# Optimization experiments

Measured on AMD Instinct MI355X. Metric: run time of the kernel, lower is better.

The kernel has to match this reference:

```python
import jax, jax.numpy as jnp
import numpy as np


def setup_inputs() -> dict:
    key = jax.random.key(0)
    k1, k2 = jax.random.split(key)
    T, D, K = 100000, 768, 500  # frames, feature dim (HuBERT base), k-means clusters
    feat = jax.random.normal(k1, (T, D), dtype=jnp.float32)
    C = jax.random.normal(k2, (D, K), dtype=jnp.float32)  # cluster centers, transposed as in module
    return {"feat": feat, "C": C}


def reference(feat, C):
    # Squared euclidean distance expanded: ||f||^2 - 2 f.C + ||c||^2
    Cnorm = jnp.sum(C * C, axis=0, keepdims=True)            # [1, K]
    fnorm = jnp.sum(feat * feat, axis=1, keepdims=True)       # [T, 1]
    dist = fnorm - 2.0 * jnp.matmul(feat, C) + Cnorm          # [T, K]
    return jnp.argmin(dist, axis=1)[None, :]                  # [1, T] cluster ids
```

## Files before the change

kernel.cpp:

```cpp
#include <hip/hip_runtime.h>
#include <float.h>

#define D_DIM 768
#define K_DIM 500
#define NDT   24
#define BM    64
#define NTH   512
#define PB_STRIDE 100352

typedef _Float16 f16x8 __attribute__((ext_vector_type(8)));
typedef _Float16 f16x4 __attribute__((ext_vector_type(4)));
typedef float    f32x4 __attribute__((ext_vector_type(4)));


__global__ void cnorm_partial_kernel(const float* __restrict__ C,
                                     double* __restrict__ partial, int K) {
    const int k = threadIdx.x;
    const int w = blockIdx.x;
    double s = 0.0;
    if (k < K) {
        const int d0 = w * (D_DIM / 16);
        for (int d = d0; d < d0 + (D_DIM / 16); ++d) {
            const float c = C[(size_t)d * K + k];
            s = fma((double)c, (double)c, s);
        }
    }
    partial[w * 512 + k] = s;
}

__global__ void cnorm_finish_kernel(const double* __restrict__ partial,
                                    float* __restrict__ cnorm, int K) {
    const int k = threadIdx.x;
    if (k < K) {
        double s = 0.0;
        for (int w = 0; w < 16; ++w) s += partial[w * 512 + k];
        cnorm[k] = (float)s;
    } else {
        cnorm[k] = FLT_MAX;
    }
}

__global__ void packB_kernel(const float* __restrict__ C,
                             _Float16* __restrict__ BpH,
                             _Float16* __restrict__ BpL) {
    const int idx = blockIdx.x * 256 + threadIdx.x;
    const int col = idx & 511;
    const int dt  = idx >> 9;
    f16x8 h[4], l[4];
    #pragma unroll
    for (int c = 0; c < 4; ++c)
        #pragma unroll
        for (int j = 0; j < 8; ++j) {
            const int k = c * 8 + j;
            const float v = (col < K_DIM)
                          ? C[(size_t)(dt * 32 + k) * K_DIM + col] : 0.0f;
            const _Float16 hh = (_Float16)v;
            h[c][j] = hh;
            l[c][j] = (_Float16)(v - (float)hh);
        }
    f16x8* dH = (f16x8*)(BpH + ((size_t)dt * 512 + col) * 32);
    f16x8* dL = (f16x8*)(BpL + ((size_t)dt * 512 + col) * 32);
    #pragma unroll
    for (int c = 0; c < 4; ++c) { dH[c] = h[c]; dL[c] = l[c]; }
}

__launch_bounds__(NTH, 4)
__global__ void assign_kernel(const float* __restrict__ feat,
                              const _Float16* __restrict__ BpH,
                              const _Float16* __restrict__ BpL,
                              const float* __restrict__ cnorm,
                              float* __restrict__ pbv,
                              int* __restrict__ pbi,
                              int T) {
    __shared__ __align__(16) _Float16 AsH[2][BM * 32];
    __shared__ __align__(16) _Float16 AsL[2][BM * 32];
    __shared__ float red_v[BM * 8];
    __shared__ int   red_i[BM * 8];

    const int tid  = threadIdx.x;
    const int wn   = tid >> 6;
    const int lane = tid & 63;
    const int l15  = lane & 15;
    const int kg   = lane >> 4;
    const int bid  = blockIdx.x;
    const int half = bid & 1;
    const int R0   = (bid >> 1) * BM;

    const int ar = tid >> 3;
    const int jj = tid & 7;
    const bool arow_ok = (R0 + ar) < T;
    const float* fptr = feat + (size_t)(R0 + ar) * D_DIM + jj * 4;
    const int aslot = (((jj >> 1) + (ar >> 1)) & 3);
    const int aoff  = ar * 32 + aslot * 8 + (jj & 1) * 4;

    const int colbase = half * 256 + wn * 32 + l15;
    const _Float16* bpH = BpH + (size_t)colbase * 32 + kg * 8;
    const _Float16* bpL = BpL + (size_t)colbase * 32 + kg * 8;

    f32x4 acc[4][2];
    #pragma unroll
    for (int m = 0; m < 4; ++m)
        #pragma unroll
        for (int n = 0; n < 2; ++n) acc[m][n] = (f32x4){0.f, 0.f, 0.f, 0.f};

#define CVT_STORE(V, BUF) do {                                                 \
    const float fa_[4] = {(V).x, (V).y, (V).z, (V).w};                         \
    f16x4 h_, l_;                                                              \
    _Pragma("unroll")                                                          \
    for (int j = 0; j < 4; ++j) {                                              \
        const _Float16 hh = (_Float16)fa_[j];                                  \
        h_[j] = hh; l_[j] = (_Float16)(fa_[j] - (float)hh);                    \
    }                                                                          \
    *(f16x4*)(AsH[BUF] + aoff) = h_;                                           \
    *(f16x4*)(AsL[BUF] + aoff) = l_;                                           \
} while (0)

#define SOFT_BARRIER() do {                                                    \
    asm volatile("s_waitcnt lgkmcnt(0)" ::: "memory");                         \
    __builtin_amdgcn_s_barrier();                                              \
} while (0)

#define BODY(DT, BCH, BCL, BNH, BNL, ACUR, ANXT) do {                          \
    const int cur = (DT) & 1;                                                  \
           \
    if ((DT) + 1 < NDT) {                                                      \
        const size_t bo1 = (size_t)((DT) + 1) * 16384;                         \
        BNH[0] = *(const f16x8*)(bpH + bo1);                                   \
        BNH[1] = *(const f16x8*)(bpH + bo1 + 512);                             \
        BNL[0] = *(const f16x8*)(bpL + bo1);                                   \
        BNL[1] = *(const f16x8*)(bpL + bo1 + 512);                             \
    }                                                                          \
                                                     \
    if ((DT) + 2 < NDT && arow_ok) {                                           \
        ANXT = *(const float4*)(fptr + ((DT) + 2) * 32);                       \
    }                                                                          \
                                            \
    f16x8 aH[4], aL[4];                                                        \
    _Pragma("unroll")                                                          \
    for (int m = 0; m < 4; ++m) {                                              \
        const int row = m * 16 + l15;                                          \
        const int sl  = (kg + (row >> 1)) & 3;                                 \
        aH[m] = ((const f16x8*)AsH[cur])[row * 4 + sl];                        \
        aL[m] = ((const f16x8*)AsL[cur])[row * 4 + sl];                        \
    }                                                                          \
         \
    __builtin_amdgcn_s_setprio(1);                                             \
    _Pragma("unroll")                                                          \
    for (int nh = 0; nh < 2; ++nh)                                             \
        _Pragma("unroll")                                                      \
        for (int m = 0; m < 4; ++m) {                                          \
            f32x4 a = acc[m][nh];                                              \
            a = __builtin_amdgcn_mfma_f32_16x16x32_f16(aH[m], BCH[nh], a, 0, 0, 0); \
            a = __builtin_amdgcn_mfma_f32_16x16x32_f16(aL[m], BCH[nh], a, 0, 0, 0); \
            a = __builtin_amdgcn_mfma_f32_16x16x32_f16(aH[m], BCL[nh], a, 0, 0, 0); \
            acc[m][nh] = a;                                                    \
        }                                                                      \
    __builtin_amdgcn_s_setprio(0);                                             \
                  \
    if ((DT) + 1 < NDT) {                                                      \
        CVT_STORE(ACUR, cur ^ 1);                                              \
    }                                                                          \
    SOFT_BARRIER();                                                            \
} while (0)

    {
        float4 v = make_float4(0.f, 0.f, 0.f, 0.f);
        if (arow_ok) v = *(const float4*)(fptr);
        CVT_STORE(v, 0);
    }
    f16x8 bAH[2], bAL[2], bBH[2], bBL[2];
    bAH[0] = *(const f16x8*)(bpH);
    bAH[1] = *(const f16x8*)(bpH + 512);
    bAL[0] = *(const f16x8*)(bpL);
    bAL[1] = *(const f16x8*)(bpL + 512);
    float4 avA = make_float4(0.f, 0.f, 0.f, 0.f), avB = avA;
    if (arow_ok) avA = *(const float4*)(fptr + 32);
    SOFT_BARRIER();

    for (int it2 = 0; it2 < NDT; it2 += 2) {
        BODY(it2,     bAH, bAL, bBH, bBL, avA, avB);
        BODY(it2 + 1, bBH, bBL, bAH, bAL, avB, avA);
    }
#undef BODY
#undef SOFT_BARRIER
#undef CVT_STORE

    float cn[2];
    #pragma unroll
    for (int nh = 0; nh < 2; ++nh)
        cn[nh] = cnorm[half * 256 + wn * 32 + nh * 16 + l15];

    #pragma unroll
    for (int m = 0; m < 4; ++m) {
        #pragma unroll
        for (int r = 0; r < 4; ++r) {
            float best = cn[0] - 2.0f * acc[m][0][r];
            int   bi   = colbase;
            {
                const int col = colbase + 16;
                const float s = cn[1] - 2.0f * acc[m][1][r];
                if (s < best || (s == best && col < bi)) { best = s; bi = col; }
            }
            #pragma unroll
            for (int msk = 1; msk < 16; msk <<= 1) {
                const float ov = __shfl_xor(best, msk, 64);
                const int   oi = __shfl_xor(bi,   msk, 64);
                if (ov < best || (ov == best && oi < bi)) { best = ov; bi = oi; }
            }
            if (l15 == 0) {
                const int rl = m * 16 + kg * 4 + r;
                red_v[rl * 8 + wn] = best;
                red_i[rl * 8 + wn] = bi;
            }
        }
    }
    __syncthreads();

    if (tid < BM) {
        float bv = red_v[tid * 8];
        int   bi = red_i[tid * 8];
        #pragma unroll
        for (int w = 1; w < 8; ++w) {
            const float v = red_v[tid * 8 + w];
            const int   i = red_i[tid * 8 + w];
            if (v < bv || (v == bv && i < bi)) { bv = v; bi = i; }
        }
        const int r = R0 + tid;
        if (r < T) {
            pbv[(size_t)half * PB_STRIDE + r] = bv;
            pbi[(size_t)half * PB_STRIDE + r] = bi;
        }
    }
}

__global__ void combine_kernel(const float* __restrict__ pbv,
                               const int* __restrict__ pbi,
                               int* __restrict__ out, int T) {
    const int r = blockIdx.x * 256 + threadIdx.x;
    if (r < T) {
        const float s0 = pbv[r];
        const int   i0 = pbi[r];
        const float s1 = pbv[PB_STRIDE + r];
        const int   i1 = pbi[PB_STRIDE + r];
        out[r] = (s1 < s0) ? i1 : i0;
    }
}

extern "C" void kernel_launch(void* const* d_in, const int* in_sizes, int n_in,
                              void* d_out, int out_size, void* d_ws, size_t ws_size,
                              hipStream_t stream) {
    const float* feat = (const float*)d_in[0];
    const float* C    = (const float*)d_in[1];
    int* out          = (int*)d_out;
    const int T = in_sizes[0] / D_DIM;
    const int K = in_sizes[1] / D_DIM;

    float*     cnorm   = (float*)d_ws;
    double*    partial = (double*)((char*)d_ws + 4096);
    _Float16*  BpH     = (_Float16*)((char*)d_ws + 131072);
    _Float16*  BpL     = (_Float16*)((char*)d_ws + 917504);
    float*     pbv     = (float*)((char*)d_ws + 1703936);
    int*       pbi     = (int*)((char*)d_ws + 2506752);

    hipLaunchKernelGGL(cnorm_partial_kernel, dim3(16), dim3(512), 0, stream,
                       C, partial, K);
    hipLaunchKernelGGL(cnorm_finish_kernel, dim3(1), dim3(512), 0, stream,
                       partial, cnorm, K);
    hipLaunchKernelGGL(packB_kernel, dim3(48), dim3(256), 0, stream,
                       C, BpH, BpL);

    const int nrb = (T + BM - 1) / BM;
    hipLaunchKernelGGL(assign_kernel, dim3(nrb * 2), dim3(NTH), 0, stream,
                       feat, BpH, BpL, cnorm, pbv, pbi, T);
    hipLaunchKernelGGL(combine_kernel, dim3((T + 255) / 256), dim3(256), 0, stream,
                       pbv, pbi, out, T);
}
```

Before: 297.5 us.

## Cover all 512 columns per block, drop column split and combine kernel

Each block now handles all 512 padded centroid columns (each wave 64 columns, 4 MFMA column tiles) instead of splitting columns across two blocks. This halves redundant feature loads and fp16 split conversions per row and removes the partial-result buffers and the separate combine kernel launch. B fragments are now loaded within the same iteration instead of being prefetched one step ahead, and the occupancy hint drops from 4 to 3 blocks per CU because the larger accumulator array needs more registers. Both changes may expose B load latency.

New measurement: 342.5 us. +15.1%, slower.

```diff
diff --git a/kernel.cpp b/kernel.cpp
--- a/kernel.cpp
+++ b/kernel.cpp
@@ -6,7 +6,6 @@
 #define NDT   24
 #define BM    64
 #define NTH   512
-#define PB_STRIDE 100352
 
 typedef _Float16 f16x8 __attribute__((ext_vector_type(8)));
 typedef _Float16 f16x4 __attribute__((ext_vector_type(4)));
@@ -64,13 +63,12 @@
     for (int c = 0; c < 4; ++c) { dH[c] = h[c]; dL[c] = l[c]; }
 }
 
-__launch_bounds__(NTH, 4)
+__launch_bounds__(NTH, 3)
 __global__ void assign_kernel(const float* __restrict__ feat,
                               const _Float16* __restrict__ BpH,
                               const _Float16* __restrict__ BpL,
                               const float* __restrict__ cnorm,
-                              float* __restrict__ pbv,
-                              int* __restrict__ pbi,
+                              int* __restrict__ out,
                               int T) {
     __shared__ __align__(16) _Float16 AsH[2][BM * 32];
     __shared__ __align__(16) _Float16 AsL[2][BM * 32];
@@ -82,9 +80,7 @@
     const int lane = tid & 63;
     const int l15  = lane & 15;
     const int kg   = lane >> 4;
-    const int bid  = blockIdx.x;
-    const int half = bid & 1;
-    const int R0   = (bid >> 1) * BM;
+    const int R0   = blockIdx.x * BM;
 
     const int ar = tid >> 3;
     const int jj = tid & 7;
@@ -93,15 +89,15 @@
     const int aslot = (((jj >> 1) + (ar >> 1)) & 3);
     const int aoff  = ar * 32 + aslot * 8 + (jj & 1) * 4;
 
-    const int colbase = half * 256 + wn * 32 + l15;
+    const int colbase = wn * 64 + l15;
     const _Float16* bpH = BpH + (size_t)colbase * 32 + kg * 8;
     const _Float16* bpL = BpL + (size_t)colbase * 32 + kg * 8;
 
-    f32x4 acc[4][2];
+    f32x4 acc[4][4];
     #pragma unroll
     for (int m = 0; m < 4; ++m)
         #pragma unroll
-        for (int n = 0; n < 2; ++n) acc[m][n] = (f32x4){0.f, 0.f, 0.f, 0.f};
+        for (int n = 0; n < 4; ++n) acc[m][n] = (f32x4){0.f, 0.f, 0.f, 0.f};
 
 #define CVT_STORE(V, BUF) do {                                                 \
     const float fa_[4] = {(V).x, (V).y, (V).z, (V).w};                         \
@@ -120,19 +116,20 @@
     __builtin_amdgcn_s_barrier();                                              \
 } while (0)
 
-#define BODY(DT, BCH, BCL, BNH, BNL, ACUR, ANXT) do {                          \
+#define BODY(DT, CUR, NXT) do {                                                \
     const int cur = (DT) & 1;                                                  \
-           \
-    if ((DT) + 1 < NDT) {                                                      \
-        const size_t bo1 = (size_t)((DT) + 1) * 16384;                         \
-        BNH[0] = *(const f16x8*)(bpH + bo1);                                   \
-        BNH[1] = *(const f16x8*)(bpH + bo1 + 512);                             \
-        BNL[0] = *(const f16x8*)(bpL + bo1);                                   \
-        BNL[1] = *(const f16x8*)(bpL + bo1 + 512);                             \
-    }                                                                          \
-                                                     \
+         \
+       \
+    const size_t bo = (size_t)(DT) * 16384;                                    \
+    f16x8 bH[4], bL[4];                                                        \
+    _Pragma("unroll")                                                          \
+    for (int nh = 0; nh < 4; ++nh) {                                           \
+        bH[nh] = *(const f16x8*)(bpH + bo + nh * 512);                         \
+        bL[nh] = *(const f16x8*)(bpL + bo + nh * 512);                         \
+    }                                                                          \
+          \
     if ((DT) + 2 < NDT && arow_ok) {                                           \
-        ANXT = *(const float4*)(fptr + ((DT) + 2) * 32);                       \
+        NXT = *(const float4*)(fptr + ((DT) + 2) * 32);                        \
     }                                                                          \
                                             \
     f16x8 aH[4], aL[4];                                                        \
@@ -143,22 +140,21 @@
         aH[m] = ((const f16x8*)AsH[cur])[row * 4 + sl];                        \
         aL[m] = ((const f16x8*)AsL[cur])[row * 4 + sl];                        \
     }                                                                          \
-         \
     __builtin_amdgcn_s_setprio(1);                                             \
     _Pragma("unroll")                                                          \
-    for (int nh = 0; nh < 2; ++nh)                                             \
+    for (int nh = 0; nh < 4; ++nh)                                             \
         _Pragma("unroll")                                                      \
         for (int m = 0; m < 4; ++m) {                                          \
             f32x4 a = acc[m][nh];                                              \
-            a = __builtin_amdgcn_mfma_f32_16x16x32_f16(aH[m], BCH[nh], a, 0, 0, 0); \
-            a = __builtin_amdgcn_mfma_f32_16x16x32_f16(aL[m], BCH[nh], a, 0, 0, 0); \
-            a = __builtin_amdgcn_mfma_f32_16x16x32_f16(aH[m], BCL[nh], a, 0, 0, 0); \
+            a = __builtin_amdgcn_mfma_f32_16x16x32_f16(aH[m], bH[nh], a, 0, 0, 0); \
+            a = __builtin_amdgcn_mfma_f32_16x16x32_f16(aL[m], bH[nh], a, 0, 0, 0); \
+            a = __builtin_amdgcn_mfma_f32_16x16x32_f16(aH[m], bL[nh], a, 0, 0, 0); \
             acc[m][nh] = a;                                                    \
         }                                                                      \
     __builtin_amdgcn_s_setprio(0);                                             \
-                  \
+       \
     if ((DT) + 1 < NDT) {                                                      \
-        CVT_STORE(ACUR, cur ^ 1);                                              \
+        CVT_STORE(CUR, cur ^ 1);                                               \
     }                                                                          \
     SOFT_BARRIER();                                                            \
 } while (0)
@@ -168,27 +164,22 @@
         if (arow_ok) v = *(const float4*)(fptr);
         CVT_STORE(v, 0);
     }
-    f16x8 bAH[2], bAL[2], bBH[2], bBL[2];
-    bAH[0] = *(const f16x8*)(bpH);
-    bAH[1] = *(const f16x8*)(bpH + 512);
-    bAL[0] = *(const f16x8*)(bpL);
-    bAL[1] = *(const f16x8*)(bpL + 512);
-    float4 avA = make_float4(0.f, 0.f, 0.f, 0.f), avB = avA;
-    if (arow_ok) avA = *(const float4*)(fptr + 32);
-    SOFT_BARRIER();
+    float4 pa = make_float4(0.f, 0.f, 0.f, 0.f), pb = pa;
+    if (arow_ok) pa = *(const float4*)(fptr + 32);
+    __syncthreads();
 
     for (int it2 = 0; it2 < NDT; it2 += 2) {
-        BODY(it2,     bAH, bAL, bBH, bBL, avA, avB);
-        BODY(it2 + 1, bBH, bBL, bAH, bAL, avB, avA);
+        BODY(it2,     pa, pb);
+        BODY(it2 + 1, pb, pa);
     }
 #undef BODY
 #undef SOFT_BARRIER
 #undef CVT_STORE
 
-    float cn[2];
-    #pragma unroll
-    for (int nh = 0; nh < 2; ++nh)
-        cn[nh] = cnorm[half * 256 + wn * 32 + nh * 16 + l15];
+    float cn[4];
+    #pragma unroll
+    for (int nh = 0; nh < 4; ++nh)
+        cn[nh] = cnorm[wn * 64 + nh * 16 + l15];
 
     #pragma unroll
     for (int m = 0; m < 4; ++m) {
@@ -196,9 +187,10 @@
         for (int r = 0; r < 4; ++r) {
             float best = cn[0] - 2.0f * acc[m][0][r];
             int   bi   = colbase;
-            {
-                const int col = colbase + 16;
-                const float s = cn[1] - 2.0f * acc[m][1][r];
+            #pragma unroll
+            for (int nh = 1; nh < 4; ++nh) {
+                const int col = colbase + nh * 16;
+                const float s = cn[nh] - 2.0f * acc[m][nh][r];
                 if (s < best || (s == best && col < bi)) { best = s; bi = col; }
             }
             #pragma unroll
@@ -226,23 +218,7 @@
             if (v < bv || (v == bv && i < bi)) { bv = v; bi = i; }
         }
         const int r = R0 + tid;
-        if (r < T) {
-            pbv[(size_t)half * PB_STRIDE + r] = bv;
-            pbi[(size_t)half * PB_STRIDE + r] = bi;
-        }
-    }
-}
-
-__global__ void combine_kernel(const float* __restrict__ pbv,
-                               const int* __restrict__ pbi,
-                               int* __restrict__ out, int T) {
-    const int r = blockIdx.x * 256 + threadIdx.x;
-    if (r < T) {
-        const float s0 = pbv[r];
-        const int   i0 = pbi[r];
-        const float s1 = pbv[PB_STRIDE + r];
-        const int   i1 = pbi[PB_STRIDE + r];
-        out[r] = (s1 < s0) ? i1 : i0;
+        if (r < T) out[r] = bi;
     }
 }
 
@@ -259,8 +235,6 @@
     double*    partial = (double*)((char*)d_ws + 4096);
     _Float16*  BpH     = (_Float16*)((char*)d_ws + 131072);
     _Float16*  BpL     = (_Float16*)((char*)d_ws + 917504);
-    float*     pbv     = (float*)((char*)d_ws + 1703936);
-    int*       pbi     = (int*)((char*)d_ws + 2506752);
 
     hipLaunchKernelGGL(cnorm_partial_kernel, dim3(16), dim3(512), 0, stream,
                        C, partial, K);
@@ -270,8 +244,6 @@
                        C, BpH, BpL);
 
     const int nrb = (T + BM - 1) / BM;
-    hipLaunchKernelGGL(assign_kernel, dim3(nrb * 2), dim3(NTH), 0, stream,
-                       feat, BpH, BpL, cnorm, pbv, pbi, T);
-    hipLaunchKernelGGL(combine_kernel, dim3((T + 255) / 256), dim3(256), 0, stream,
-                       pbv, pbi, out, T);
-}
+    hipLaunchKernelGGL(assign_kernel, dim3(nrb), dim3(NTH), 0, stream,
+                       feat, BpH, BpL, cnorm, out, T);
+}
```
